# Performance work log

Hardware: AMD Instinct MI355X
Metric: run time of the kernel (lower is better)

Reference implementation:

```python
import jax, jax.numpy as jnp
import numpy as np

NEG = -9e15   # mask value used by reference pyGAT implementation
ALPHA = 0.2   # LeakyReLU negative slope
B, N, F_IN, H, F_HID = 131072, 8, 30, 3, 8


def setup_inputs() -> dict:
    key = jax.random.key(0)
    ks = jax.random.split(key, 14)
    x = jax.random.normal(ks[0], (B, N, F_IN), jnp.float32)
    adj = (jax.random.uniform(ks[1], (B, N, N)) > 0.5).astype(jnp.float32)
    adj = jnp.maximum(adj, jnp.eye(N, dtype=jnp.float32))  # self loops

    def init(k, shp, fan):
        return jax.random.normal(k, shp, jnp.float32) * np.float32(1.0 / np.sqrt(fan))

    return {
        "x": x,
        "adj": adj,
        "W_heads": init(ks[2], (H, F_IN, F_HID), F_IN),       # per-head W
        "a_heads": init(ks[3], (H, 2 * F_HID), 2 * F_HID),    # per-head attention vec
        "W_out": init(ks[4], (H * F_HID, 1), H * F_HID),      # out_att W (nclass=1)
        "a_out": init(ks[5], (2,), 2),                          # out_att attention vec
        "mu_W": init(ks[6], (8, 8), 8), "mu_b": jnp.zeros((8,), jnp.float32),
        "sg_W": init(ks[7], (8, 8), 8), "sg_b": jnp.zeros((8,), jnp.float32),
        "v_W": init(ks[8], (1, 8), 8), "v_b": jnp.zeros((1,), jnp.float32),
    }


def _gat(x, adj, W_heads, a_heads, W_out, a_out):
    # --- multi-head layer (concat=True) ---
    Wh = jnp.einsum('bnf,hfo->bhno', x, W_heads)            # [B,H,N,F_HID]
    a1, a2 = a_heads[:, :F_HID], a_heads[:, F_HID:]
    f1 = jnp.einsum('bhno,ho->bhn', Wh, a1)
    f2 = jnp.einsum('bhno,ho->bhn', Wh, a2)
    e = jax.nn.leaky_relu(f1[:, :, :, None] + f2[:, :, None, :], ALPHA)  # [B,H,N,N]
    e = jnp.where(adj[:, None, :, :] > 0, e, NEG)
    att = jax.nn.softmax(e, axis=-1)
    h = jax.nn.elu(jnp.einsum('bhnm,bhmo->bhno', att, Wh))  # [B,H,N,F_HID]
    h = h.transpose(0, 2, 1, 3).reshape(x.shape[0], N, H * F_HID)  # concat heads

    # --- output attention layer (concat=False, nclass=1) ---
    Wh2 = h @ W_out                                          # [B,N,1]
    g1 = Wh2[..., 0] * a_out[0]
    g2 = Wh2[..., 0] * a_out[1]
    e2 = jax.nn.leaky_relu(g1[:, :, None] + g2[:, None, :], ALPHA)  # [B,N,N]
    e2 = jnp.where(adj > 0, e2, NEG)
    att2 = jax.nn.softmax(e2, axis=-1)
    out = jnp.einsum('bnm,bmo->bno', att2, Wh2)              # [B,N,1]
    return jax.nn.elu(out)[..., 0]                            # squeeze(-1) -> [B,8]


def reference(x, adj, W_heads, a_heads, W_out, a_out,
              mu_W, mu_b, sg_W, sg_b, v_W, v_b):
    g = _gat(x, adj, W_heads, a_heads, W_out, a_out)          # [B,8]
    mu = jax.nn.sigmoid(g @ mu_W.T + mu_b)                    # [B,8]
    sigma = jax.nn.softplus(g @ sg_W.T + sg_b) + 0.001        # [B,8]
    value = g @ v_W.T + v_b                                   # [B,1]
    return (mu, sigma, value)
```

## Files before the change

### kernel.cpp

```cpp
#include <hip/hip_runtime.h>
#include <math.h>

#define TPB 256

constexpr int Bn    = 131072;
constexpr float LOG2E = 1.4426950408889634f;

typedef float v2f __attribute__((ext_vector_type(2)));

__global__ __launch_bounds__(TPB)
void gat_ppo_kernel(const float* __restrict__ xg,
                    const float* __restrict__ adjg,
                    const float* __restrict__ Wg,
                    const float* __restrict__ ahg,
                    const float* __restrict__ wog,
                    const float* __restrict__ aog,
                    const float* __restrict__ muWg,
                    const float* __restrict__ mubg,
                    const float* __restrict__ sgWg,
                    const float* __restrict__ sgbg,
                    const float* __restrict__ vWg,
                    const float* __restrict__ vbg,
                    float* __restrict__ outg)
{
    __shared__ float4 tile[4 * 200];

    const int lb = threadIdx.x;
    const int w  = lb >> 6;
    const int g  = (lb & 63) >> 3;
    const int n  = lb & 7;
    const int t  = blockIdx.x * TPB + lb;

    float4* wt4 = tile + w * 200;

    unsigned amask;
    {
        const float4* a4 = (const float4*)(adjg) + (size_t)t * 2;
        float4 a0 = a4[0], a1 = a4[1];
        amask =  (unsigned)(a0.x > 0.0f)
              | ((unsigned)(a0.y > 0.0f) << 1)
              | ((unsigned)(a0.z > 0.0f) << 2)
              | ((unsigned)(a0.w > 0.0f) << 3)
              | ((unsigned)(a1.x > 0.0f) << 4)
              | ((unsigned)(a1.y > 0.0f) << 5)
              | ((unsigned)(a1.z > 0.0f) << 6)
              | ((unsigned)(a1.w > 0.0f) << 7);
    }

    float x[30];
    {
        const float2* xr = (const float2*)(xg + (size_t)t * 30);
        #pragma unroll
        for (int k = 0; k < 15; ++k) {
            float2 v = xr[k];
            x[2 * k] = v.x; x[2 * k + 1] = v.y;
        }
    }

    const v2f* Wp = (const v2f*)Wg;
    float wh2 = 0.0f;

    #pragma unroll
    for (int h = 0; h < 3; ++h) {
        v2f acc[4];
        #pragma unroll
        for (int o2 = 0; o2 < 4; ++o2) acc[o2] = (v2f){0.0f, 0.0f};
        #pragma unroll
        for (int f = 0; f < 30; ++f) {
            v2f xf = (v2f){x[f], x[f]};
            #pragma unroll
            for (int o2 = 0; o2 < 4; ++o2)
                acc[o2] = __builtin_elementwise_fma(xf, Wp[h * 120 + f * 4 + o2], acc[o2]);
        }

        float s1 = 0.0f, s2 = 0.0f;
        #pragma unroll
        for (int o2 = 0; o2 < 4; ++o2) {
            s1 = fmaf(acc[o2].x, ahg[h * 16 + 2 * o2],     s1);
            s1 = fmaf(acc[o2].y, ahg[h * 16 + 2 * o2 + 1], s1);
            s2 = fmaf(acc[o2].x, ahg[h * 16 + 8 + 2 * o2],     s2);
            s2 = fmaf(acc[o2].y, ahg[h * 16 + 8 + 2 * o2 + 1], s2);
        }
        float f1h = s1 * LOG2E;
        float f2h = s2 * LOG2E;

        wt4[g * 25 + n * 3]     = (float4){acc[0].x, acc[0].y, acc[1].x, acc[1].y};
        wt4[g * 25 + n * 3 + 1] = (float4){acc[2].x, acc[2].y, acc[3].x, acc[3].y};

        float p[8];
        float s = 0.0f;
        #pragma unroll
        for (int m = 0; m < 8; ++m) {
            float ev = f1h + __shfl(f2h, m, 8);
            ev = fmaxf(ev, 0.2f * ev);
            float pe = ((amask >> m) & 1u) ? __builtin_amdgcn_exp2f(ev) : 0.0f;
            p[m] = pe; s += pe;
        }

        v2f hacc[4];
        #pragma unroll
        for (int o2 = 0; o2 < 4; ++o2) hacc[o2] = (v2f){0.0f, 0.0f};
        #pragma unroll
        for (int m = 0; m < 8; ++m) {
            float4 lo = wt4[g * 25 + m * 3];
            float4 hi = wt4[g * 25 + m * 3 + 1];
            v2f av = (v2f){p[m], p[m]};
            hacc[0] = __builtin_elementwise_fma(av, (v2f){lo.x, lo.y}, hacc[0]);
            hacc[1] = __builtin_elementwise_fma(av, (v2f){lo.z, lo.w}, hacc[1]);
            hacc[2] = __builtin_elementwise_fma(av, (v2f){hi.x, hi.y}, hacc[2]);
            hacc[3] = __builtin_elementwise_fma(av, (v2f){hi.z, hi.w}, hacc[3]);
        }
        float rs = 1.0f / s;
        #pragma unroll
        for (int o2 = 0; o2 < 4; ++o2) {
            #pragma unroll
            for (int j = 0; j < 2; ++j) {
                float hv = hacc[o2][j] * rs;
                hv = (hv > 0.0f) ? hv : (__expf(hv) - 1.0f);
                wh2 = fmaf(hv, wog[h * 8 + 2 * o2 + j], wh2);
            }
        }
    }

    const float a0c = aog[0] * LOG2E, a1c = aog[1] * LOG2E;
    float wh2a[8];
    #pragma unroll
    for (int m = 0; m < 8; ++m) wh2a[m] = __shfl(wh2, m, 8);

    float g1 = a0c * wh2;
    float s2s = 0.0f;
    float og = 0.0f;
    #pragma unroll
    for (int m = 0; m < 8; ++m) {
        float ev = fmaf(a1c, wh2a[m], g1);
        ev = fmaxf(ev, 0.2f * ev);
        float pe = ((amask >> m) & 1u) ? __builtin_amdgcn_exp2f(ev) : 0.0f;
        s2s += pe;
        og = fmaf(pe, wh2a[m], og);
    }
    og /= s2s;
    float g2v = (og > 0.0f) ? og : (__expf(og) - 1.0f);

    v2f gp[4];
    #pragma unroll
    for (int m = 0; m < 4; ++m)
        gp[m] = (v2f){__shfl(g2v, 2 * m, 8), __shfl(g2v, 2 * m + 1, 8)};

    const v2f* muWp = (const v2f*)muWg;
    const v2f* sgWp = (const v2f*)sgWg;
    const v2f* vWp  = (const v2f*)vWg;
    v2f ma = (v2f){0.0f, 0.0f}, sa = (v2f){0.0f, 0.0f}, va = (v2f){0.0f, 0.0f};
    #pragma unroll
    for (int k = 0; k < 4; ++k) {
        ma = __builtin_elementwise_fma(gp[k], muWp[n * 4 + k], ma);
        sa = __builtin_elementwise_fma(gp[k], sgWp[n * 4 + k], sa);
        va = __builtin_elementwise_fma(gp[k], vWp[k],          va);
    }
    float mu = ma.x + ma.y + mubg[n];
    float sg = sa.x + sa.y + sgbg[n];
    float vv = va.x + va.y + vbg[0];

    mu = 1.0f / (1.0f + __expf(-mu));
    sg = fmaxf(sg, 0.0f) + log1pf(__expf(-fabsf(sg))) + 0.001f;

    outg[t]          = mu;
    outg[Bn * 8 + t] = sg;
    if (n == 0) outg[Bn * 16 + (t >> 3)] = vv;
}

extern "C" void kernel_launch(void* const* d_in, const int* in_sizes, int n_in,
                              void* d_out, int out_size, void* d_ws, size_t ws_size,
                              hipStream_t stream) {
    const float* xg   = (const float*)d_in[0];
    const float* adjg = (const float*)d_in[1];
    const float* Wg   = (const float*)d_in[2];
    const float* ahg  = (const float*)d_in[3];
    const float* wog  = (const float*)d_in[4];
    const float* aog  = (const float*)d_in[5];
    const float* muW  = (const float*)d_in[6];
    const float* mub  = (const float*)d_in[7];
    const float* sgW  = (const float*)d_in[8];
    const float* sgb  = (const float*)d_in[9];
    const float* vW   = (const float*)d_in[10];
    const float* vb   = (const float*)d_in[11];
    float* outg = (float*)d_out;

    dim3 grid(Bn * 8 / TPB);
    gat_ppo_kernel<<<grid, TPB, 0, stream>>>(xg, adjg, Wg, ahg, wog, aog,
                                             muW, mub, sgW, sgb, vW, vb, outg);
}
```

Measured before the change: 50.37 us.

## Process two node rows per thread to reuse weight loads across graphs

```diff
diff --git a/kernel.cpp b/kernel.cpp
--- a/kernel.cpp
+++ b/kernel.cpp
@@ -8,7 +8,7 @@
 
 typedef float v2f __attribute__((ext_vector_type(2)));
 
-__global__ __launch_bounds__(TPB)
+__global__ __launch_bounds__(TPB, 4)
 void gat_ppo_kernel(const float* __restrict__ xg,
                     const float* __restrict__ adjg,
                     const float* __restrict__ Wg,
@@ -23,149 +23,184 @@
                     const float* __restrict__ vbg,
                     float* __restrict__ outg)
 {
-    __shared__ float4 tile[4 * 200];
+    __shared__ float4 tile[4 * 2 * 200];
 
     const int lb = threadIdx.x;
     const int w  = lb >> 6;
     const int g  = (lb & 63) >> 3;
     const int n  = lb & 7;
-    const int t  = blockIdx.x * TPB + lb;
-
-    float4* wt4 = tile + w * 200;
-
-    unsigned amask;
-    {
-        const float4* a4 = (const float4*)(adjg) + (size_t)t * 2;
+    const size_t rbase = (size_t)blockIdx.x * (2 * TPB) + lb;
+
+    float4* wtA = tile + w * 400;
+    float4* wtB = wtA + 200;
+
+    unsigned amask[2];
+    float x[2][30];
+    #pragma unroll
+    for (int q = 0; q < 2; ++q) {
+        const size_t r = rbase + q * TPB;
+        const float4* a4 = (const float4*)(adjg) + r * 2;
         float4 a0 = a4[0], a1 = a4[1];
-        amask =  (unsigned)(a0.x > 0.0f)
-              | ((unsigned)(a0.y > 0.0f) << 1)
-              | ((unsigned)(a0.z > 0.0f) << 2)
-              | ((unsigned)(a0.w > 0.0f) << 3)
-              | ((unsigned)(a1.x > 0.0f) << 4)
-              | ((unsigned)(a1.y > 0.0f) << 5)
-              | ((unsigned)(a1.z > 0.0f) << 6)
-              | ((unsigned)(a1.w > 0.0f) << 7);
-    }
-
-    float x[30];
-    {
-        const float2* xr = (const float2*)(xg + (size_t)t * 30);
+        amask[q] =  (unsigned)(a0.x > 0.0f)
+                 | ((unsigned)(a0.y > 0.0f) << 1)
+                 | ((unsigned)(a0.z > 0.0f) << 2)
+                 | ((unsigned)(a0.w > 0.0f) << 3)
+                 | ((unsigned)(a1.x > 0.0f) << 4)
+                 | ((unsigned)(a1.y > 0.0f) << 5)
+                 | ((unsigned)(a1.z > 0.0f) << 6)
+                 | ((unsigned)(a1.w > 0.0f) << 7);
+        const float2* xr = (const float2*)(xg + r * 30);
         #pragma unroll
         for (int k = 0; k < 15; ++k) {
             float2 v = xr[k];
-            x[2 * k] = v.x; x[2 * k + 1] = v.y;
+            x[q][2 * k] = v.x; x[q][2 * k + 1] = v.y;
         }
     }
 
     const v2f* Wp = (const v2f*)Wg;
-    float wh2 = 0.0f;
+    float wh2[2] = {0.0f, 0.0f};
 
     #pragma unroll
     for (int h = 0; h < 3; ++h) {
-        v2f acc[4];
-        #pragma unroll
-        for (int o2 = 0; o2 < 4; ++o2) acc[o2] = (v2f){0.0f, 0.0f};
+        v2f acc[2][4];
+        #pragma unroll
+        for (int q = 0; q < 2; ++q)
+            #pragma unroll
+            for (int o2 = 0; o2 < 4; ++o2) acc[q][o2] = (v2f){0.0f, 0.0f};
+
         #pragma unroll
         for (int f = 0; f < 30; ++f) {
-            v2f xf = (v2f){x[f], x[f]};
-            #pragma unroll
-            for (int o2 = 0; o2 < 4; ++o2)
-                acc[o2] = __builtin_elementwise_fma(xf, Wp[h * 120 + f * 4 + o2], acc[o2]);
-        }
-
-        float s1 = 0.0f, s2 = 0.0f;
-        #pragma unroll
-        for (int o2 = 0; o2 < 4; ++o2) {
-            s1 = fmaf(acc[o2].x, ahg[h * 16 + 2 * o2],     s1);
-            s1 = fmaf(acc[o2].y, ahg[h * 16 + 2 * o2 + 1], s1);
-            s2 = fmaf(acc[o2].x, ahg[h * 16 + 8 + 2 * o2],     s2);
-            s2 = fmaf(acc[o2].y, ahg[h * 16 + 8 + 2 * o2 + 1], s2);
-        }
-        float f1h = s1 * LOG2E;
-        float f2h = s2 * LOG2E;
-
-        wt4[g * 25 + n * 3]     = (float4){acc[0].x, acc[0].y, acc[1].x, acc[1].y};
-        wt4[g * 25 + n * 3 + 1] = (float4){acc[2].x, acc[2].y, acc[3].x, acc[3].y};
-
-        float p[8];
-        float s = 0.0f;
+            #pragma unroll
+            for (int o2 = 0; o2 < 4; ++o2) {
+                v2f wv = Wp[h * 120 + f * 4 + o2];
+                acc[0][o2] = __builtin_elementwise_fma((v2f){x[0][f], x[0][f]}, wv, acc[0][o2]);
+                acc[1][o2] = __builtin_elementwise_fma((v2f){x[1][f], x[1][f]}, wv, acc[1][o2]);
+            }
+        }
+
+        float f1h[2], f2h[2];
+        #pragma unroll
+        for (int q = 0; q < 2; ++q) {
+            float s1 = 0.0f, s2 = 0.0f;
+            #pragma unroll
+            for (int o2 = 0; o2 < 4; ++o2) {
+                s1 = fmaf(acc[q][o2].x, ahg[h * 16 + 2 * o2],     s1);
+                s1 = fmaf(acc[q][o2].y, ahg[h * 16 + 2 * o2 + 1], s1);
+                s2 = fmaf(acc[q][o2].x, ahg[h * 16 + 8 + 2 * o2],     s2);
+                s2 = fmaf(acc[q][o2].y, ahg[h * 16 + 8 + 2 * o2 + 1], s2);
+            }
+            f1h[q] = s1 * LOG2E;
+            f2h[q] = s2 * LOG2E;
+        }
+
+        wtA[g * 25 + n * 3]     = (float4){acc[0][0].x, acc[0][0].y, acc[0][1].x, acc[0][1].y};
+        wtA[g * 25 + n * 3 + 1] = (float4){acc[0][2].x, acc[0][2].y, acc[0][3].x, acc[0][3].y};
+        wtB[g * 25 + n * 3]     = (float4){acc[1][0].x, acc[1][0].y, acc[1][1].x, acc[1][1].y};
+        wtB[g * 25 + n * 3 + 1] = (float4){acc[1][2].x, acc[1][2].y, acc[1][3].x, acc[1][3].y};
+
+        float p[2][8];
+        float s[2] = {0.0f, 0.0f};
         #pragma unroll
         for (int m = 0; m < 8; ++m) {
-            float ev = f1h + __shfl(f2h, m, 8);
+            #pragma unroll
+            for (int q = 0; q < 2; ++q) {
+                float ev = f1h[q] + __shfl(f2h[q], m, 8);
+                ev = fmaxf(ev, 0.2f * ev);
+                float pe = ((amask[q] >> m) & 1u) ? __builtin_amdgcn_exp2f(ev) : 0.0f;
+                p[q][m] = pe; s[q] += pe;
+            }
+        }
+
+        v2f hacc[2][4];
+        #pragma unroll
+        for (int q = 0; q < 2; ++q)
+            #pragma unroll
+            for (int o2 = 0; o2 < 4; ++o2) hacc[q][o2] = (v2f){0.0f, 0.0f};
+
+        #pragma unroll
+        for (int m = 0; m < 8; ++m) {
+            float4 loA = wtA[g * 25 + m * 3];
+            float4 hiA = wtA[g * 25 + m * 3 + 1];
+            float4 loB = wtB[g * 25 + m * 3];
+            float4 hiB = wtB[g * 25 + m * 3 + 1];
+            v2f avA = (v2f){p[0][m], p[0][m]};
+            v2f avB = (v2f){p[1][m], p[1][m]};
+            hacc[0][0] = __builtin_elementwise_fma(avA, (v2f){loA.x, loA.y}, hacc[0][0]);
+            hacc[0][1] = __builtin_elementwise_fma(avA, (v2f){loA.z, loA.w}, hacc[0][1]);
+            hacc[0][2] = __builtin_elementwise_fma(avA, (v2f){hiA.x, hiA.y}, hacc[0][2]);
+            hacc[0][3] = __builtin_elementwise_fma(avA, (v2f){hiA.z, hiA.w}, hacc[0][3]);
+            hacc[1][0] = __builtin_elementwise_fma(avB, (v2f){loB.x, loB.y}, hacc[1][0]);
+            hacc[1][1] = __builtin_elementwise_fma(avB, (v2f){loB.z, loB.w}, hacc[1][1]);
+            hacc[1][2] = __builtin_elementwise_fma(avB, (v2f){hiB.x, hiB.y}, hacc[1][2]);
+            hacc[1][3] = __builtin_elementwise_fma(avB, (v2f){hiB.z, hiB.w}, hacc[1][3]);
+        }
+
+        #pragma unroll
+        for (int q = 0; q < 2; ++q) {
+            float rs = 1.0f / s[q];
+            #pragma unroll
+            for (int o2 = 0; o2 < 4; ++o2) {
+                #pragma unroll
+                for (int j = 0; j < 2; ++j) {
+                    float hv = hacc[q][o2][j] * rs;
+                    hv = (hv > 0.0f) ? hv : (__expf(hv) - 1.0f);
+                    wh2[q] = fmaf(hv, wog[h * 8 + 2 * o2 + j], wh2[q]);
+                }
+            }
+        }
+    }
+
+    const float a0c = aog[0] * LOG2E, a1c = aog[1] * LOG2E;
+    float g2v[2];
+    #pragma unroll
+    for (int q = 0; q < 2; ++q) {
+        float wh2a[8];
+        #pragma unroll
+        for (int m = 0; m < 8; ++m) wh2a[m] = __shfl(wh2[q], m, 8);
+
+        float g1 = a0c * wh2[q];
+        float s2s = 0.0f, og = 0.0f;
+        #pragma unroll
+        for (int m = 0; m < 8; ++m) {
+            float ev = fmaf(a1c, wh2a[m], g1);
             ev = fmaxf(ev, 0.2f * ev);
-            float pe = ((amask >> m) & 1u) ? __builtin_amdgcn_exp2f(ev) : 0.0f;
-            p[m] = pe; s += pe;
-        }
-
-        v2f hacc[4];
-        #pragma unroll
-        for (int o2 = 0; o2 < 4; ++o2) hacc[o2] = (v2f){0.0f, 0.0f};
-        #pragma unroll
-        for (int m = 0; m < 8; ++m) {
-            float4 lo = wt4[g * 25 + m * 3];
-            float4 hi = wt4[g * 25 + m * 3 + 1];
-            v2f av = (v2f){p[m], p[m]};
-            hacc[0] = __builtin_elementwise_fma(av, (v2f){lo.x, lo.y}, hacc[0]);
-            hacc[1] = __builtin_elementwise_fma(av, (v2f){lo.z, lo.w}, hacc[1]);
-            hacc[2] = __builtin_elementwise_fma(av, (v2f){hi.x, hi.y}, hacc[2]);
-            hacc[3] = __builtin_elementwise_fma(av, (v2f){hi.z, hi.w}, hacc[3]);
-        }
-        float rs = 1.0f / s;
-        #pragma unroll
-        for (int o2 = 0; o2 < 4; ++o2) {
-            #pragma unroll
-            for (int j = 0; j < 2; ++j) {
-                float hv = hacc[o2][j] * rs;
-                hv = (hv > 0.0f) ? hv : (__expf(hv) - 1.0f);
-                wh2 = fmaf(hv, wog[h * 8 + 2 * o2 + j], wh2);
-            }
-        }
-    }
-
-    const float a0c = aog[0] * LOG2E, a1c = aog[1] * LOG2E;
-    float wh2a[8];
-    #pragma unroll
-    for (int m = 0; m < 8; ++m) wh2a[m] = __shfl(wh2, m, 8);
-
-    float g1 = a0c * wh2;
-    float s2s = 0.0f;
-    float og = 0.0f;
-    #pragma unroll
-    for (int m = 0; m < 8; ++m) {
-        float ev = fmaf(a1c, wh2a[m], g1);
-        ev = fmaxf(ev, 0.2f * ev);
-        float pe = ((amask >> m) & 1u) ? __builtin_amdgcn_exp2f(ev) : 0.0f;
-        s2s += pe;
-        og = fmaf(pe, wh2a[m], og);
-    }
-    og /= s2s;
-    float g2v = (og > 0.0f) ? og : (__expf(og) - 1.0f);
-
-    v2f gp[4];
-    #pragma unroll
-    for (int m = 0; m < 4; ++m)
-        gp[m] = (v2f){__shfl(g2v, 2 * m, 8), __shfl(g2v, 2 * m + 1, 8)};
+            float pe = ((amask[q] >> m) & 1u) ? __builtin_amdgcn_exp2f(ev) : 0.0f;
+            s2s += pe;
+            og = fmaf(pe, wh2a[m], og);
+        }
+        og /= s2s;
+        g2v[q] = (og > 0.0f) ? og : (__expf(og) - 1.0f);
+    }
 
     const v2f* muWp = (const v2f*)muWg;
     const v2f* sgWp = (const v2f*)sgWg;
     const v2f* vWp  = (const v2f*)vWg;
-    v2f ma = (v2f){0.0f, 0.0f}, sa = (v2f){0.0f, 0.0f}, va = (v2f){0.0f, 0.0f};
-    #pragma unroll
-    for (int k = 0; k < 4; ++k) {
-        ma = __builtin_elementwise_fma(gp[k], muWp[n * 4 + k], ma);
-        sa = __builtin_elementwise_fma(gp[k], sgWp[n * 4 + k], sa);
-        va = __builtin_elementwise_fma(gp[k], vWp[k],          va);
-    }
-    float mu = ma.x + ma.y + mubg[n];
-    float sg = sa.x + sa.y + sgbg[n];
-    float vv = va.x + va.y + vbg[0];
-
-    mu = 1.0f / (1.0f + __expf(-mu));
-    sg = fmaxf(sg, 0.0f) + log1pf(__expf(-fabsf(sg))) + 0.001f;
-
-    outg[t]          = mu;
-    outg[Bn * 8 + t] = sg;
-    if (n == 0) outg[Bn * 16 + (t >> 3)] = vv;
+    #pragma unroll
+    for (int q = 0; q < 2; ++q) {
+        v2f gp[4];
+        #pragma unroll
+        for (int m = 0; m < 4; ++m)
+            gp[m] = (v2f){__shfl(g2v[q], 2 * m, 8), __shfl(g2v[q], 2 * m + 1, 8)};
+
+        v2f ma = (v2f){0.0f, 0.0f}, sa = (v2f){0.0f, 0.0f}, va = (v2f){0.0f, 0.0f};
+        #pragma unroll
+        for (int k = 0; k < 4; ++k) {
+            ma = __builtin_elementwise_fma(gp[k], muWp[n * 4 + k], ma);
+            sa = __builtin_elementwise_fma(gp[k], sgWp[n * 4 + k], sa);
+            va = __builtin_elementwise_fma(gp[k], vWp[k],          va);
+        }
+        float mu = ma.x + ma.y + mubg[n];
+        float sg = sa.x + sa.y + sgbg[n];
+        float vv = va.x + va.y + vbg[0];
+
+        mu = 1.0f / (1.0f + __expf(-mu));
+        sg = fmaxf(sg, 0.0f) + log1pf(__expf(-fabsf(sg))) + 0.001f;
+
+        const size_t r = rbase + q * TPB;
+        outg[r]          = mu;
+        outg[Bn * 8 + r] = sg;
+        if (n == 0) outg[Bn * 16 + (r >> 3)] = vv;
+    }
 }
 
 extern "C" void kernel_launch(void* const* d_in, const int* in_sizes, int n_in,
@@ -185,7 +220,7 @@
     const float* vb   = (const float*)d_in[11];
     float* outg = (float*)d_out;
 
-    dim3 grid(Bn * 8 / TPB);
+    dim3 grid(Bn * 8 / (2 * TPB));
     gat_ppo_kernel<<<grid, TPB, 0, stream>>>(xg, adjg, Wg, ahg, wog, aog,
                                              muW, mub, sgW, sgb, vW, vb, outg);
 }
```

Result: slower. 71.37 us (+41.7%).

## Map one graph per thread instead of one node per thread

Applied to the files above, without the earlier changes.

```diff
diff --git a/kernel.cpp b/kernel.cpp
--- a/kernel.cpp
+++ b/kernel.cpp
@@ -23,149 +23,157 @@
                     const float* __restrict__ vbg,
                     float* __restrict__ outg)
 {
-    __shared__ float4 tile[4 * 200];
+    const size_t b = (size_t)blockIdx.x * TPB + threadIdx.x;
 
-    const int lb = threadIdx.x;
-    const int w  = lb >> 6;
-    const int g  = (lb & 63) >> 3;
-    const int n  = lb & 7;
-    const int t  = blockIdx.x * TPB + lb;
-
-    float4* wt4 = tile + w * 200;
-
-    unsigned amask;
+    unsigned long long am = 0ull;
     {
-        const float4* a4 = (const float4*)(adjg) + (size_t)t * 2;
-        float4 a0 = a4[0], a1 = a4[1];
-        amask =  (unsigned)(a0.x > 0.0f)
-              | ((unsigned)(a0.y > 0.0f) << 1)
-              | ((unsigned)(a0.z > 0.0f) << 2)
-              | ((unsigned)(a0.w > 0.0f) << 3)
-              | ((unsigned)(a1.x > 0.0f) << 4)
-              | ((unsigned)(a1.y > 0.0f) << 5)
-              | ((unsigned)(a1.z > 0.0f) << 6)
-              | ((unsigned)(a1.w > 0.0f) << 7);
-    }
-
-    float x[30];
-    {
-        const float2* xr = (const float2*)(xg + (size_t)t * 30);
+        const float4* a4 = (const float4*)(adjg + b * 64);
         #pragma unroll
-        for (int k = 0; k < 15; ++k) {
-            float2 v = xr[k];
-            x[2 * k] = v.x; x[2 * k + 1] = v.y;
+        for (int i = 0; i < 16; ++i) {
+            float4 v = a4[i];
+            am |= ((unsigned long long)(v.x > 0.0f)) << (4 * i + 0);
+            am |= ((unsigned long long)(v.y > 0.0f)) << (4 * i + 1);
+            am |= ((unsigned long long)(v.z > 0.0f)) << (4 * i + 2);
+            am |= ((unsigned long long)(v.w > 0.0f)) << (4 * i + 3);
         }
     }
 
-    const v2f* Wp = (const v2f*)Wg;
-    float wh2 = 0.0f;
+    const v2f* Wp  = (const v2f*)Wg;
+    const float* xb = xg + b * (8 * 30);
 
+    float wh2[8];
     #pragma unroll
+    for (int n = 0; n < 8; ++n) wh2[n] = 0.0f;
+
+    #pragma unroll 1
     for (int h = 0; h < 3; ++h) {
-        v2f acc[4];
+        const v2f*   Whp = Wp + h * 120;
+        const float* ah1 = ahg + h * 16;
+        const float* ah2 = ahg + h * 16 + 8;
+        const float* woh = wog + h * 8;
+
+        v2f   wh[8][4];
+        float f1[8], f2[8];
+
         #pragma unroll
-        for (int o2 = 0; o2 < 4; ++o2) acc[o2] = (v2f){0.0f, 0.0f};
-        #pragma unroll
-        for (int f = 0; f < 30; ++f) {
-            v2f xf = (v2f){x[f], x[f]};
+        for (int n = 0; n < 8; ++n) {
+            const float4* x4 = (const float4*)(xb + n * 30);
+            float4 c0 = x4[0], c1 = x4[1], c2 = x4[2], c3 = x4[3];
+            float4 c4 = x4[4], c5 = x4[5], c6 = x4[6];
+            float2 c7 = ((const float2*)(xb + n * 30))[14];
+            const float xv[30] = {c0.x,c0.y,c0.z,c0.w, c1.x,c1.y,c1.z,c1.w,
+                                  c2.x,c2.y,c2.z,c2.w, c3.x,c3.y,c3.z,c3.w,
+                                  c4.x,c4.y,c4.z,c4.w, c5.x,c5.y,c5.z,c5.w,
+                                  c6.x,c6.y,c6.z,c6.w, c7.x,c7.y};
+            v2f acc0 = (v2f){0.0f,0.0f}, acc1 = (v2f){0.0f,0.0f};
+            v2f acc2 = (v2f){0.0f,0.0f}, acc3 = (v2f){0.0f,0.0f};
             #pragma unroll
-            for (int o2 = 0; o2 < 4; ++o2)
-                acc[o2] = __builtin_elementwise_fma(xf, Wp[h * 120 + f * 4 + o2], acc[o2]);
+            for (int f = 0; f < 30; ++f) {
+                v2f xf = (v2f){xv[f], xv[f]};
+                acc0 = __builtin_elementwise_fma(xf, Whp[f * 4 + 0], acc0);
+                acc1 = __builtin_elementwise_fma(xf, Whp[f * 4 + 1], acc1);
+                acc2 = __builtin_elementwise_fma(xf, Whp[f * 4 + 2], acc2);
+                acc3 = __builtin_elementwise_fma(xf, Whp[f * 4 + 3], acc3);
+            }
+            wh[n][0] = acc0; wh[n][1] = acc1; wh[n][2] = acc2; wh[n][3] = acc3;
+
+            float s1 = 0.0f, s2 = 0.0f;
+            s1 = fmaf(acc0.x, ah1[0], s1); s1 = fmaf(acc0.y, ah1[1], s1);
+            s1 = fmaf(acc1.x, ah1[2], s1); s1 = fmaf(acc1.y, ah1[3], s1);
+            s1 = fmaf(acc2.x, ah1[4], s1); s1 = fmaf(acc2.y, ah1[5], s1);
+            s1 = fmaf(acc3.x, ah1[6], s1); s1 = fmaf(acc3.y, ah1[7], s1);
+            s2 = fmaf(acc0.x, ah2[0], s2); s2 = fmaf(acc0.y, ah2[1], s2);
+            s2 = fmaf(acc1.x, ah2[2], s2); s2 = fmaf(acc1.y, ah2[3], s2);
+            s2 = fmaf(acc2.x, ah2[4], s2); s2 = fmaf(acc2.y, ah2[5], s2);
+            s2 = fmaf(acc3.x, ah2[6], s2); s2 = fmaf(acc3.y, ah2[7], s2);
+            f1[n] = s1 * LOG2E;
+            f2[n] = s2 * LOG2E;
         }
 
-        float s1 = 0.0f, s2 = 0.0f;
         #pragma unroll
-        for (int o2 = 0; o2 < 4; ++o2) {
-            s1 = fmaf(acc[o2].x, ahg[h * 16 + 2 * o2],     s1);
-            s1 = fmaf(acc[o2].y, ahg[h * 16 + 2 * o2 + 1], s1);
-            s2 = fmaf(acc[o2].x, ahg[h * 16 + 8 + 2 * o2],     s2);
-            s2 = fmaf(acc[o2].y, ahg[h * 16 + 8 + 2 * o2 + 1], s2);
-        }
-        float f1h = s1 * LOG2E;
-        float f2h = s2 * LOG2E;
-
-        wt4[g * 25 + n * 3]     = (float4){acc[0].x, acc[0].y, acc[1].x, acc[1].y};
-        wt4[g * 25 + n * 3 + 1] = (float4){acc[2].x, acc[2].y, acc[3].x, acc[3].y};
-
-        float p[8];
-        float s = 0.0f;
-        #pragma unroll
-        for (int m = 0; m < 8; ++m) {
-            float ev = f1h + __shfl(f2h, m, 8);
-            ev = fmaxf(ev, 0.2f * ev);
-            float pe = ((amask >> m) & 1u) ? __builtin_amdgcn_exp2f(ev) : 0.0f;
-            p[m] = pe; s += pe;
-        }
-
-        v2f hacc[4];
-        #pragma unroll
-        for (int o2 = 0; o2 < 4; ++o2) hacc[o2] = (v2f){0.0f, 0.0f};
-        #pragma unroll
-        for (int m = 0; m < 8; ++m) {
-            float4 lo = wt4[g * 25 + m * 3];
-            float4 hi = wt4[g * 25 + m * 3 + 1];
-            v2f av = (v2f){p[m], p[m]};
-            hacc[0] = __builtin_elementwise_fma(av, (v2f){lo.x, lo.y}, hacc[0]);
-            hacc[1] = __builtin_elementwise_fma(av, (v2f){lo.z, lo.w}, hacc[1]);
-            hacc[2] = __builtin_elementwise_fma(av, (v2f){hi.x, hi.y}, hacc[2]);
-            hacc[3] = __builtin_elementwise_fma(av, (v2f){hi.z, hi.w}, hacc[3]);
-        }
-        float rs = 1.0f / s;
-        #pragma unroll
-        for (int o2 = 0; o2 < 4; ++o2) {
+        for (int n = 0; n < 8; ++n) {
+            float s = 0.0f;
+            v2f hacc0 = (v2f){0.0f,0.0f}, hacc1 = (v2f){0.0f,0.0f};
+            v2f hacc2 = (v2f){0.0f,0.0f}, hacc3 = (v2f){0.0f,0.0f};
             #pragma unroll
-            for (int j = 0; j < 2; ++j) {
-                float hv = hacc[o2][j] * rs;
-                hv = (hv > 0.0f) ? hv : (__expf(hv) - 1.0f);
-                wh2 = fmaf(hv, wog[h * 8 + 2 * o2 + j], wh2);
+            for (int m = 0; m < 8; ++m) {
+                float ev = f1[n] + f2[m];
+                ev = fmaxf(ev, 0.2f * ev);
+                float pe = ((am >> (n * 8 + m)) & 1ull)
+                         ? __builtin_amdgcn_exp2f(ev) : 0.0f;
+                s += pe;
+                v2f av = (v2f){pe, pe};
+                hacc0 = __builtin_elementwise_fma(av, wh[m][0], hacc0);
+                hacc1 = __builtin_elementwise_fma(av, wh[m][1], hacc1);
+                hacc2 = __builtin_elementwise_fma(av, wh[m][2], hacc2);
+                hacc3 = __builtin_elementwise_fma(av, wh[m][3], hacc3);
             }
+            float rs = 1.0f / s;
+            float hv;
+            hv = hacc0.x * rs; hv = (hv > 0.0f) ? hv : (__expf(hv) - 1.0f); wh2[n] = fmaf(hv, woh[0], wh2[n]);
+            hv = hacc0.y * rs; hv = (hv > 0.0f) ? hv : (__expf(hv) - 1.0f); wh2[n] = fmaf(hv, woh[1], wh2[n]);
+            hv = hacc1.x * rs; hv = (hv > 0.0f) ? hv : (__expf(hv) - 1.0f); wh2[n] = fmaf(hv, woh[2], wh2[n]);
+            hv = hacc1.y * rs; hv = (hv > 0.0f) ? hv : (__expf(hv) - 1.0f); wh2[n] = fmaf(hv, woh[3], wh2[n]);
+            hv = hacc2.x * rs; hv = (hv > 0.0f) ? hv : (__expf(hv) - 1.0f); wh2[n] = fmaf(hv, woh[4], wh2[n]);
+            hv = hacc2.y * rs; hv = (hv > 0.0f) ? hv : (__expf(hv) - 1.0f); wh2[n] = fmaf(hv, woh[5], wh2[n]);
+            hv = hacc3.x * rs; hv = (hv > 0.0f) ? hv : (__expf(hv) - 1.0f); wh2[n] = fmaf(hv, woh[6], wh2[n]);
+            hv = hacc3.y * rs; hv = (hv > 0.0f) ? hv : (__expf(hv) - 1.0f); wh2[n] = fmaf(hv, woh[7], wh2[n]);
         }
     }
 
     const float a0c = aog[0] * LOG2E, a1c = aog[1] * LOG2E;
-    float wh2a[8];
+    float g[8];
     #pragma unroll
-    for (int m = 0; m < 8; ++m) wh2a[m] = __shfl(wh2, m, 8);
-
-    float g1 = a0c * wh2;
-    float s2s = 0.0f;
-    float og = 0.0f;
-    #pragma unroll
-    for (int m = 0; m < 8; ++m) {
-        float ev = fmaf(a1c, wh2a[m], g1);
-        ev = fmaxf(ev, 0.2f * ev);
-        float pe = ((amask >> m) & 1u) ? __builtin_amdgcn_exp2f(ev) : 0.0f;
-        s2s += pe;
-        og = fmaf(pe, wh2a[m], og);
+    for (int n = 0; n < 8; ++n) {
+        float g1 = a0c * wh2[n];
+        float s2s = 0.0f, og = 0.0f;
+        #pragma unroll
+        for (int m = 0; m < 8; ++m) {
+            float ev = fmaf(a1c, wh2[m], g1);
+            ev = fmaxf(ev, 0.2f * ev);
+            float pe = ((am >> (n * 8 + m)) & 1ull)
+                     ? __builtin_amdgcn_exp2f(ev) : 0.0f;
+            s2s += pe;
+            og = fmaf(pe, wh2[m], og);
+        }
+        og /= s2s;
+        g[n] = (og > 0.0f) ? og : (__expf(og) - 1.0f);
     }
-    og /= s2s;
-    float g2v = (og > 0.0f) ? og : (__expf(og) - 1.0f);
 
     v2f gp[4];
     #pragma unroll
-    for (int m = 0; m < 4; ++m)
-        gp[m] = (v2f){__shfl(g2v, 2 * m, 8), __shfl(g2v, 2 * m + 1, 8)};
+    for (int k = 0; k < 4; ++k) gp[k] = (v2f){g[2 * k], g[2 * k + 1]};
 
     const v2f* muWp = (const v2f*)muWg;
     const v2f* sgWp = (const v2f*)sgWg;
     const v2f* vWp  = (const v2f*)vWg;
-    v2f ma = (v2f){0.0f, 0.0f}, sa = (v2f){0.0f, 0.0f}, va = (v2f){0.0f, 0.0f};
+
+    float mu[8], sg[8];
     #pragma unroll
-    for (int k = 0; k < 4; ++k) {
-        ma = __builtin_elementwise_fma(gp[k], muWp[n * 4 + k], ma);
-        sa = __builtin_elementwise_fma(gp[k], sgWp[n * 4 + k], sa);
-        va = __builtin_elementwise_fma(gp[k], vWp[k],          va);
+    for (int j = 0; j < 8; ++j) {
+        v2f ma = (v2f){0.0f,0.0f}, sa = (v2f){0.0f,0.0f};
+        #pragma unroll
+        for (int k = 0; k < 4; ++k) {
+            ma = __builtin_elementwise_fma(gp[k], muWp[j * 4 + k], ma);
+            sa = __builtin_elementwise_fma(gp[k], sgWp[j * 4 + k], sa);
+        }
+        float m = ma.x + ma.y + mubg[j];
+        float t = sa.x + sa.y + sgbg[j];
+        mu[j] = 1.0f / (1.0f + __expf(-m));
+        sg[j] = fmaxf(t, 0.0f) + log1pf(__expf(-fabsf(t))) + 0.001f;
     }
-    float mu = ma.x + ma.y + mubg[n];
-    float sg = sa.x + sa.y + sgbg[n];
+    v2f va = (v2f){0.0f,0.0f};
+    #pragma unroll
+    for (int k = 0; k < 4; ++k) va = __builtin_elementwise_fma(gp[k], vWp[k], va);
     float vv = va.x + va.y + vbg[0];
 
-    mu = 1.0f / (1.0f + __expf(-mu));
-    sg = fmaxf(sg, 0.0f) + log1pf(__expf(-fabsf(sg))) + 0.001f;
-
-    outg[t]          = mu;
-    outg[Bn * 8 + t] = sg;
-    if (n == 0) outg[Bn * 16 + (t >> 3)] = vv;
+    float4* om = (float4*)(outg + b * 8);
+    om[0] = (float4){mu[0], mu[1], mu[2], mu[3]};
+    om[1] = (float4){mu[4], mu[5], mu[6], mu[7]};
+    float4* os = (float4*)(outg + (size_t)Bn * 8 + b * 8);
+    os[0] = (float4){sg[0], sg[1], sg[2], sg[3]};
+    os[1] = (float4){sg[4], sg[5], sg[6], sg[7]};
+    outg[(size_t)Bn * 16 + b] = vv;
 }
 
 extern "C" void kernel_launch(void* const* d_in, const int* in_sizes, int n_in,
@@ -185,7 +193,7 @@
     const float* vb   = (const float*)d_in[11];
     float* outg = (float*)d_out;
 
-    dim3 grid(Bn * 8 / TPB);
+    dim3 grid(Bn / TPB);
     gat_ppo_kernel<<<grid, TPB, 0, stream>>>(xg, adjg, Wg, ahg, wog, aog,
                                              muW, mub, sgW, sgb, vW, vb, outg);
 }
```

Measured after the change: 136.2 us. 2.7x slower.

## Replace LDS tile and shuffles with DPP row-rotation ring over interleaved graphs

Applied to the files above, without the earlier changes.

```diff
diff --git a/kernel.cpp b/kernel.cpp
--- a/kernel.cpp
+++ b/kernel.cpp
@@ -7,6 +7,18 @@
 constexpr float LOG2E = 1.4426950408889634f;
 
 typedef float v2f __attribute__((ext_vector_type(2)));
+
+__device__ __forceinline__ float fror2(float v) {
+    int i = __builtin_bit_cast(int, v);
+    i = __builtin_amdgcn_update_dpp(i, i, 0x122, 0xf, 0xf, false);
+    return __builtin_bit_cast(float, i);
+}
+__device__ __forceinline__ int iror2(int v) {
+    return __builtin_amdgcn_update_dpp(v, v, 0x122, 0xf, 0xf, false);
+}
+__device__ __forceinline__ v2f vror2(v2f v) {
+    v2f o; o.x = fror2(v.x); o.y = fror2(v.y); return o;
+}
 
 __global__ __launch_bounds__(TPB)
 void gat_ppo_kernel(const float* __restrict__ xg,
@@ -23,19 +35,15 @@
                     const float* __restrict__ vbg,
                     float* __restrict__ outg)
 {
-    __shared__ float4 tile[4 * 200];
-
-    const int lb = threadIdx.x;
-    const int w  = lb >> 6;
-    const int g  = (lb & 63) >> 3;
-    const int n  = lb & 7;
-    const int t  = blockIdx.x * TPB + lb;
-
-    float4* wt4 = tile + w * 200;
+    const int lb   = threadIdx.x;
+    const int r16  = lb & 15;
+    const int par  = r16 & 1;
+    const int n    = r16 >> 1;
+    const size_t b = (size_t)blockIdx.x * 32 + (lb >> 4) * 2 + par;
 
     unsigned amask;
     {
-        const float4* a4 = (const float4*)(adjg) + (size_t)t * 2;
+        const float4* a4 = (const float4*)(adjg + b * 64 + n * 8);
         float4 a0 = a4[0], a1 = a4[1];
         amask =  (unsigned)(a0.x > 0.0f)
               | ((unsigned)(a0.y > 0.0f) << 1)
@@ -49,7 +57,7 @@
 
     float x[30];
     {
-        const float2* xr = (const float2*)(xg + (size_t)t * 30);
+        const float2* xr = (const float2*)(xg + ((size_t)b * 8 + n) * 30);
         #pragma unroll
         for (int k = 0; k < 15; ++k) {
             float2 v = xr[k];
@@ -84,38 +92,38 @@
         float f1h = s1 * LOG2E;
         float f2h = s2 * LOG2E;
 
-        wt4[g * 25 + n * 3]     = (float4){acc[0].x, acc[0].y, acc[1].x, acc[1].y};
-        wt4[g * 25 + n * 3 + 1] = (float4){acc[2].x, acc[2].y, acc[3].x, acc[3].y};
-
-        float p[8];
-        float s = 0.0f;
-        #pragma unroll
-        for (int m = 0; m < 8; ++m) {
-            float ev = f1h + __shfl(f2h, m, 8);
+        float rf2 = f2h;
+        v2f rw0 = acc[0], rw1 = acc[1], rw2 = acc[2], rw3 = acc[3];
+        int mcur = n;
+        float ssum = 0.0f;
+        v2f hacc0 = (v2f){0.0f,0.0f}, hacc1 = (v2f){0.0f,0.0f};
+        v2f hacc2 = (v2f){0.0f,0.0f}, hacc3 = (v2f){0.0f,0.0f};
+        #pragma unroll
+        for (int step = 0; step < 8; ++step) {
+            float ev = f1h + rf2;
             ev = fmaxf(ev, 0.2f * ev);
-            float pe = ((amask >> m) & 1u) ? __builtin_amdgcn_exp2f(ev) : 0.0f;
-            p[m] = pe; s += pe;
-        }
-
-        v2f hacc[4];
-        #pragma unroll
-        for (int o2 = 0; o2 < 4; ++o2) hacc[o2] = (v2f){0.0f, 0.0f};
-        #pragma unroll
-        for (int m = 0; m < 8; ++m) {
-            float4 lo = wt4[g * 25 + m * 3];
-            float4 hi = wt4[g * 25 + m * 3 + 1];
-            v2f av = (v2f){p[m], p[m]};
-            hacc[0] = __builtin_elementwise_fma(av, (v2f){lo.x, lo.y}, hacc[0]);
-            hacc[1] = __builtin_elementwise_fma(av, (v2f){lo.z, lo.w}, hacc[1]);
-            hacc[2] = __builtin_elementwise_fma(av, (v2f){hi.x, hi.y}, hacc[2]);
-            hacc[3] = __builtin_elementwise_fma(av, (v2f){hi.z, hi.w}, hacc[3]);
-        }
-        float rs = 1.0f / s;
+            float pe = ((amask >> mcur) & 1u) ? __builtin_amdgcn_exp2f(ev) : 0.0f;
+            ssum += pe;
+            v2f av = (v2f){pe, pe};
+            hacc0 = __builtin_elementwise_fma(av, rw0, hacc0);
+            hacc1 = __builtin_elementwise_fma(av, rw1, hacc1);
+            hacc2 = __builtin_elementwise_fma(av, rw2, hacc2);
+            hacc3 = __builtin_elementwise_fma(av, rw3, hacc3);
+            if (step < 7) {
+                rf2 = fror2(rf2);
+                rw0 = vror2(rw0); rw1 = vror2(rw1);
+                rw2 = vror2(rw2); rw3 = vror2(rw3);
+                mcur = iror2(mcur);
+            }
+        }
+        float rs = 1.0f / ssum;
+
+        v2f hh[4] = {hacc0, hacc1, hacc2, hacc3};
         #pragma unroll
         for (int o2 = 0; o2 < 4; ++o2) {
             #pragma unroll
             for (int j = 0; j < 2; ++j) {
-                float hv = hacc[o2][j] * rs;
+                float hv = hh[o2][j] * rs;
                 hv = (hv > 0.0f) ? hv : (__expf(hv) - 1.0f);
                 wh2 = fmaf(hv, wog[h * 8 + 2 * o2 + j], wh2);
             }
@@ -123,28 +131,33 @@
     }
 
     const float a0c = aog[0] * LOG2E, a1c = aog[1] * LOG2E;
-    float wh2a[8];
-    #pragma unroll
-    for (int m = 0; m < 8; ++m) wh2a[m] = __shfl(wh2, m, 8);
-
-    float g1 = a0c * wh2;
-    float s2s = 0.0f;
-    float og = 0.0f;
-    #pragma unroll
-    for (int m = 0; m < 8; ++m) {
-        float ev = fmaf(a1c, wh2a[m], g1);
-        ev = fmaxf(ev, 0.2f * ev);
-        float pe = ((amask >> m) & 1u) ? __builtin_amdgcn_exp2f(ev) : 0.0f;
-        s2s += pe;
-        og = fmaf(pe, wh2a[m], og);
-    }
-    og /= s2s;
-    float g2v = (og > 0.0f) ? og : (__expf(og) - 1.0f);
+    {
+        float g1 = a0c * wh2;
+        float rwh2 = wh2;
+        int mc = n;
+        float s2s = 0.0f, og = 0.0f;
+        #pragma unroll
+        for (int step = 0; step < 8; ++step) {
+            float ev = fmaf(a1c, rwh2, g1);
+            ev = fmaxf(ev, 0.2f * ev);
+            float pe = ((amask >> mc) & 1u) ? __builtin_amdgcn_exp2f(ev) : 0.0f;
+            s2s += pe;
+            og = fmaf(pe, rwh2, og);
+            if (step < 7) {
+                rwh2 = fror2(rwh2);
+                mc = iror2(mc);
+            }
+        }
+        og /= s2s;
+        wh2 = (og > 0.0f) ? og : (__expf(og) - 1.0f);
+    }
+    const float g2v = wh2;
 
     v2f gp[4];
     #pragma unroll
-    for (int m = 0; m < 4; ++m)
-        gp[m] = (v2f){__shfl(g2v, 2 * m, 8), __shfl(g2v, 2 * m + 1, 8)};
+    for (int k = 0; k < 4; ++k)
+        gp[k] = (v2f){__shfl(g2v, 4 * k + par,     16),
+                      __shfl(g2v, 4 * k + 2 + par, 16)};
 
     const v2f* muWp = (const v2f*)muWg;
     const v2f* sgWp = (const v2f*)sgWg;
@@ -163,9 +176,9 @@
     mu = 1.0f / (1.0f + __expf(-mu));
     sg = fmaxf(sg, 0.0f) + log1pf(__expf(-fabsf(sg))) + 0.001f;
 
-    outg[t]          = mu;
-    outg[Bn * 8 + t] = sg;
-    if (n == 0) outg[Bn * 16 + (t >> 3)] = vv;
+    outg[b * 8 + n]                    = mu;
+    outg[(size_t)Bn * 8 + b * 8 + n]   = sg;
+    if (n == 0) outg[(size_t)Bn * 16 + b] = vv;
 }
 
 extern "C" void kernel_launch(void* const* d_in, const int* in_sizes, int n_in,
@@ -185,7 +198,7 @@
     const float* vb   = (const float*)d_in[11];
     float* outg = (float*)d_out;
 
-    dim3 grid(Bn * 8 / TPB);
+    dim3 grid(Bn / 32);
     gat_ppo_kernel<<<grid, TPB, 0, stream>>>(xg, adjg, Wg, ahg, wog, aog,
                                              muW, mub, sgW, sgb, vW, vb, outg);
 }
```

Result: slower. 56.28 us (+11.7%).
